# Performance work log

Measured on AMD Instinct MI355X. Metric: run time of the kernel, lower is better.

## Reference

```python
import jax, jax.numpy as jnp
import numpy as np
jax.config.update("jax_enable_x64", True)

B, S, E, H, L, FF = 2, 1024, 768, 12, 4, 2048
MAX_THOUGHT_LEN = 3
LN_EPS = 1e-5

def _sinusoidal_pe(max_len, d):
    pos = np.arange(max_len)[:, None]
    div = np.exp(np.arange(0, d, 2) * (-np.log(10000.0) / d))
    pe = np.zeros((max_len, d), np.float32)
    pe[:, 0::2] = np.sin(pos * div)
    pe[:, 1::2] = np.cos(pos * div)
    return jnp.asarray(pe)

def _build_mask(Smax, thoughts_taken, n_tokens):
    # Vectorized equivalent of the torch loop building the block-causal mask.
    bs = thoughts_taken + 1
    i = np.arange(Smax)[:, None]
    j = np.arange(Smax)[None, :]
    same_block = (i // bs == j // bs) & (i // bs < n_tokens) & ((i % bs) >= (j % bs))
    start_vis = ((j % bs) == 0) & (j // bs < n_tokens) & (i > j) & (i < n_tokens * bs)
    allowed = same_block | start_vis
    # TransformerEncoder canonicalizes the bool mask: True (disallowed) -> -inf additive
    return jnp.asarray(np.where(allowed, 0.0, -np.inf).astype(np.float64))

def _layernorm(x, w, b):
    mu = jnp.mean(x, -1, keepdims=True)
    var = jnp.mean((x - mu) ** 2, -1, keepdims=True)
    return (x - mu) / jnp.sqrt(var + LN_EPS) * w + b

def setup_inputs() -> dict:
    key = jax.random.key(0)
    ks = jax.random.split(key, 8)
    f32 = jnp.float32
    return {
        "x": jax.random.normal(ks[0], (B, S, E), f32),
        "padding_mask": jnp.zeros((B, S), bool),
        "thought_pe": jax.random.normal(ks[1], (MAX_THOUGHT_LEN + 1, E), f32),
        "Wqkv": jax.random.normal(ks[2], (L, 3 * E, E), f32) * (E ** -0.5),
        "bqkv": jnp.zeros((L, 3 * E), f32),
        "W1": jax.random.normal(ks[3], (L, FF, E), f32) * (E ** -0.5),
        "b1": jnp.zeros((L, FF), f32),
        "W2": jax.random.normal(ks[4], (L, E, FF), f32) * (FF ** -0.5),
        "b2": jnp.zeros((L, E), f32),
        "ln1_w": jnp.ones((L, E), f32), "ln1_b": jnp.zeros((L, E), f32),
        "ln2_w": jnp.ones((L, E), f32), "ln2_b": jnp.zeros((L, E), f32),
        "lnf_w": jnp.ones((E,), f32), "lnf_b": jnp.zeros((E,), f32),
        "thoughts_taken": 1,
        "real_token_count": 512,
    }

def reference(x, padding_mask, thought_pe, Wqkv, bqkv, W1, b1, W2, b2,
              ln1_w, ln1_b, ln2_w, ln2_b, lnf_w, lnf_b,
              thoughts_taken, real_token_count):
    # NOTE: padding_mask is accepted but unused, matching the custom layer.
    nt = thoughts_taken + 1
    pe = _sinusoidal_pe(S, E)
    # DualPositionalEncoding (eval mode -> dropout is identity)
    h = x[:, : real_token_count * nt].reshape(B, real_token_count, nt, E)
    h = h + pe[:real_token_count][None, :, None, :] + thought_pe[:nt][None, None, :, :]
    h = h.reshape(B, real_token_count * nt, E)
    pad = S - real_token_count * nt
    if pad > 0:
        h = jnp.pad(h, ((0, 0), (0, pad), (0, 0)))
    mask = _build_mask(S, thoughts_taken, real_token_count)
    scale = 1.0 / jnp.sqrt(jnp.float64(E // H))
    for l in range(L):
        # manual fp64 attention, exactly as the torch layer
        s64 = h.astype(jnp.float64)
        qkv = s64 @ Wqkv[l].astype(jnp.float64).T + bqkv[l].astype(jnp.float64)
        q, k, v = jnp.split(qkv, 3, axis=-1)
        rh = lambda t: t.reshape(B, S, H, E // H).transpose(0, 2, 1, 3)
        q, k, v = rh(q), rh(k), rh(v)
        scores = jnp.einsum("bhqd,bhkd->bhqk", q, k) * scale + mask
        attn = jax.nn.softmax(scores, axis=-1)
        ao = jnp.einsum("bhqk,bhkd->bhqd", attn, v).transpose(0, 2, 1, 3).reshape(B, S, E)
        # NOTE: no out_proj -- the custom forward skips self_attn.out_proj
        h = _layernorm(h + ao.astype(h.dtype), ln1_w[l], ln1_b[l])
        ff = jax.nn.gelu(h @ W1[l].T + b1[l], approximate=False) @ W2[l].T + b2[l]
        h = _layernorm(h + ff, ln2_w[l], ln2_b[l])
        h = jnp.nan_to_num(h)
    return _layernorm(h, lnf_w, lnf_b)
```

## Files before the change

kernel.cpp:

```cpp
#include <hip/hip_runtime.h>
#include <math.h>

#define SEQ 1024
#define EMB 768
#define NHEAD 12
#define HDIM 64
#define NLAYER 4
#define FFDIM 2048
#define BATCH 2
#define ROWS (BATCH * SEQ)
#define BH (BATCH * NHEAD)
#define NCHUNK 2
#define CTILES 8

using f16 = _Float16;
using f16x4 = __attribute__((ext_vector_type(4))) _Float16;
using f16x8 = __attribute__((ext_vector_type(8))) _Float16;
using f32x4 = __attribute__((ext_vector_type(4))) float;
using f32x16 = __attribute__((ext_vector_type(16))) float;
typedef unsigned long long u64;

__device__ inline void gload16(const void* g, void* l) {
    __builtin_amdgcn_global_load_lds((const __attribute__((address_space(1))) unsigned*)g,
                                     (__attribute__((address_space(3))) unsigned*)l, 16, 0, 0);
}

__global__ void prep_kernel(const float* __restrict__ Wq, int na,
                            const float* __restrict__ W1, int nb,
                            const float* __restrict__ W2, int nc,
                            f16* __restrict__ oq, f16* __restrict__ o1, f16* __restrict__ o2,
                            const float* __restrict__ x,
                            const float* __restrict__ tpe,
                            float* __restrict__ h32,
                            f16* __restrict__ h16,
                            u64* __restrict__ mtab,
                            const int* __restrict__ tt_p,
                            const int* __restrict__ rtc_p) {
    const int ncast = na + nb + nc;
    const int nembed = BATCH * SEQ * EMB;
    const int nmask = SEQ * 16;
    const int total = ncast + nembed + nmask;
    const int nt = *tt_p + 1;
    const int rtc = *rtc_p;
    for (int i = blockIdx.x * blockDim.x + threadIdx.x; i < total;
         i += gridDim.x * blockDim.x) {
        if (i < ncast) {
            const float* src;
            f16* dst;
            int off;
            if (i < na)            { src = Wq; dst = oq; off = i; }
            else if (i < na + nb)  { src = W1; dst = o1; off = i - na; }
            else                   { src = W2; dst = o2; off = i - na - nb; }
            float4 v = ((const float4*)src)[off];
            f16x4 o;
            o[0] = (f16)v.x; o[1] = (f16)v.y; o[2] = (f16)v.z; o[3] = (f16)v.w;
            ((f16x4*)dst)[off] = o;
        } else if (i < ncast + nembed) {
            int idx = i - ncast;
            int e = idx % EMB;
            int s = (idx / EMB) % SEQ;
            float val;
            if (s < rtc * nt) {
                int p = s / nt;
                int t = s % nt;
                int i2 = e & ~1;
                float div = __expf((float)i2 * -0.0119926314f);
                float ang = (float)p * div;
                float pe = (e & 1) ? __cosf(ang) : __sinf(ang);
                val = x[idx] + pe + tpe[t * EMB + e];
            } else {
                val = 0.0f;
            }
            h32[idx] = val;
            h16[idx] = (f16)val;
        } else {
            int idx = i - ncast - nembed;
            int ii = idx >> 4, jt = idx & 15;
            int id = ii / nt, im = ii % nt;
            int iok = (ii < rtc * nt);
            u64 m = 0;
            for (int k = 0; k < 64; k++) {
                int j = jt * 64 + k;
                int jd = j / nt, jm = j % nt;
                bool same = (id == jd) && (id < rtc) && (im >= jm);
                bool sv   = (jm == 0) && (jd < rtc) && (ii > j) && iok;
                if (same || sv) m |= (1ull << k);
            }
            mtab[idx] = m;
        }
    }
}

template<int ACT, int OUT>
__global__ __launch_bounds__(512) void gemm_f16(const f16* __restrict__ A,
                                                const f16* __restrict__ W,
                                                const float* __restrict__ bias,
                                                f16* __restrict__ Ch,
                                                f16* __restrict__ vtg,
                                                int M, int N, int K) {
    __shared__ f16 As[2][128 * 64];
    __shared__ f16 Ws[2][128 * 64];
    const int tid = threadIdx.x, lane = tid & 63, wave = tid >> 6;
    const int gx = gridDim.x;
    const int nwg = gx * gridDim.y;
    int orig = blockIdx.y * gx + blockIdx.x;
    int nid = (nwg & 7) ? orig : ((orig & 7) * (nwg >> 3) + (orig >> 3));
    const int bm = (nid / gx) * 128, bn = (nid % gx) * 128;
    const int l31 = lane & 31, l32 = lane >> 5;
    const int wm = (wave >> 1) * 32, wn = (wave & 1) * 64;
    const int srow = lane >> 3, sslot = lane & 7;
    const int klen = K / gridDim.z;
    const int kbeg = blockIdx.z * klen;
    const int nsteps = klen >> 6;

    f32x16 acc[2];
#pragma unroll
    for (int ni = 0; ni < 2; ni++)
#pragma unroll
        for (int e = 0; e < 16; e++) acc[ni][e] = 0.f;

#pragma unroll
    for (int i = 0; i < 2; i++) {
        int R0 = wave * 16 + i * 8;
        int row = R0 + srow;
        int gs = (sslot ^ (row & 7)) << 3;
        gload16(A + (size_t)(bm + row) * K + kbeg + gs, As[0] + R0 * 64);
        gload16(W + (size_t)(bn + row) * K + kbeg + gs, Ws[0] + R0 * 64);
    }
    __syncthreads();

    int cur = 0;
    for (int t = 0; t < nsteps; t++) {
        if (t + 1 < nsteps) {
            int k1 = kbeg + (t + 1) * 64;
            int nxt = cur ^ 1;
#pragma unroll
            for (int i = 0; i < 2; i++) {
                int R0 = wave * 16 + i * 8;
                int row = R0 + srow;
                int gs = (sslot ^ (row & 7)) << 3;
                gload16(A + (size_t)(bm + row) * K + k1 + gs, As[nxt] + R0 * 64);
                gload16(W + (size_t)(bn + row) * K + k1 + gs, Ws[nxt] + R0 * 64);
            }
        }
#pragma unroll
        for (int ks = 0; ks < 4; ks++) {
            int kslot = ks * 2 + l32;
            f16x8 a, b[2];
            {
                int row = wm + l31;
                a = *(const f16x8*)(As[cur] + row * 64 + ((kslot ^ (row & 7)) << 3));
            }
#pragma unroll
            for (int ni = 0; ni < 2; ni++) {
                int row = wn + ni * 32 + l31;
                b[ni] = *(const f16x8*)(Ws[cur] + row * 64 + ((kslot ^ (row & 7)) << 3));
            }
#pragma unroll
            for (int ni = 0; ni < 2; ni++)
                acc[ni] = __builtin_amdgcn_mfma_f32_32x32x16_f16(a, b[ni], acc[ni], 0, 0, 0);
        }
        __syncthreads();
        cur ^= 1;
    }

#pragma unroll
    for (int ni = 0; ni < 2; ni++) {
        int nbase = bn + wn + ni * 32;
        int n = nbase + l31;
        if (OUT == 3) {
            f16* dst = Ch + (size_t)blockIdx.z * ROWS * N;
#pragma unroll
            for (int reg = 0; reg < 16; reg++) {
                int m = bm + wm + (reg & 3) + 8 * (reg >> 2) + 4 * l32;
                dst[(size_t)m * N + n] = (f16)acc[ni][reg];
            }
        } else {
            float bv = bias[n];
            if (OUT != 2 || nbase < 2 * EMB) {
                int cstride = (OUT == 2) ? 2 * EMB : N;
#pragma unroll
                for (int reg = 0; reg < 16; reg++) {
                    int m = bm + wm + (reg & 3) + 8 * (reg >> 2) + 4 * l32;
                    float v = acc[ni][reg] + bv;
                    if (ACT) v = 0.5f * v * (1.0f + erff(v * 0.70710678118654752f));
                    Ch[(size_t)m * cstride + n] = (f16)v;
                }
            } else {
                int d = n - 2 * EMB;
                int hh = d >> 6, dd = d & 63;
#pragma unroll
                for (int q = 0; q < 4; q++) {
                    int m0 = bm + wm + 8 * q + 4 * l32;
                    int bb = m0 >> 10, s0 = m0 & (SEQ - 1);
                    f16x4 pack;
#pragma unroll
                    for (int r = 0; r < 4; r++) pack[r] = (f16)(acc[ni][4 * q + r] + bv);
                    *(f16x4*)(vtg + ((size_t)((bb * NHEAD + hh) * HDIM + dd)) * SEQ + s0) = pack;
                }
            }
        }
    }
}

__global__ __launch_bounds__(256) void attn_part(const f16* __restrict__ qk,
                                                 const f16* __restrict__ vtg,
                                                 const u64* __restrict__ mtab,
                                                 f16* __restrict__ po,
                                                 float* __restrict__ pm,
                                                 float* __restrict__ pl) {
    const int c = blockIdx.x;
    const int qt = gridDim.y - 1 - blockIdx.y;
    if (c * CTILES > qt) return;
    const int bh = blockIdx.z;
    const int b = bh / NHEAD, hh = bh % NHEAD;
    const int q0 = qt * 64;
    const int jt_beg = c * CTILES, jt_end = min(qt, c * CTILES + CTILES - 1);

    __shared__ f16 Qs[64 * 64];
    __shared__ f16 Ks[2][64 * 64];
    __shared__ f16 VT[2][64 * 64];
    __shared__ f16 Ps[4 * 16 * 64];

    const int tid = threadIdx.x, lane = tid & 63, wave = tid >> 6;
    const int l15 = lane & 15, l16 = lane >> 4;
    const int RS = 2 * EMB;
    const f16* vth = vtg + (size_t)(b * NHEAD + hh) * HDIM * SEQ;
    const float SCALE2 = 0.125f * 1.44269504088896f;

#pragma unroll
    for (int it = 0; it < 2; it++) {
        int R0 = wave * 16 + it * 8;
        int row = R0 + (lane >> 3), slot = lane & 7;
        int gs = (slot ^ (row & 7)) << 3;
        gload16(qk + (size_t)(b * SEQ + q0 + row) * RS + hh * HDIM + gs, Qs + R0 * 64);
        gload16(qk + (size_t)(b * SEQ + jt_beg * 64 + row) * RS + EMB + hh * HDIM + gs,
                Ks[0] + R0 * 64);
        gload16(vth + (size_t)row * SEQ + jt_beg * 64 + gs, VT[0] + R0 * 64);
    }
    __syncthreads();

    f16x8 qa[2];
#pragma unroll
    for (int ks = 0; ks < 2; ks++) {
        int row = wave * 16 + l15;
        int kslot = l16 + ks * 4;
        qa[ks] = *(const f16x8*)(Qs + row * 64 + ((kslot ^ (row & 7)) << 3));
    }

    f16x8 ones;
#pragma unroll
    for (int i = 0; i < 8; i++) ones[i] = (f16)1.0f;

    float mrow[4];
    f32x4 o[4], osum;
    int iglob[4];
#pragma unroll
    for (int r = 0; r < 4; r++) {
        mrow[r] = -1e30f;
        iglob[r] = q0 + wave * 16 + l16 * 4 + r;
    }
#pragma unroll
    for (int nf = 0; nf < 4; nf++) o[nf] = (f32x4){0.f, 0.f, 0.f, 0.f};
    osum = (f32x4){0.f, 0.f, 0.f, 0.f};

    for (int jt = jt_beg; jt <= jt_end; jt++) {
        const int cur = (jt - jt_beg) & 1;
        if (jt < jt_end) {
            const int nxt = cur ^ 1;
            const int jn0 = (jt + 1) * 64;
#pragma unroll
            for (int it = 0; it < 2; it++) {
                int R0 = wave * 16 + it * 8;
                int row = R0 + (lane >> 3), slot = lane & 7;
                int gs = (slot ^ (row & 7)) << 3;
                gload16(qk + (size_t)(b * SEQ + jn0 + row) * RS + EMB + hh * HDIM + gs,
                        Ks[nxt] + R0 * 64);
                gload16(vth + (size_t)row * SEQ + jn0 + gs, VT[nxt] + R0 * 64);
            }
        }

        unsigned mlo[4], mhi[4];
#pragma unroll
        for (int r = 0; r < 4; r++) {
            u64 mk = mtab[iglob[r] * 16 + jt];
            mlo[r] = (unsigned)mk;
            mhi[r] = (unsigned)(mk >> 32);
        }

        f32x4 s[4];
        __builtin_amdgcn_s_setprio(1);
#pragma unroll
        for (int nf = 0; nf < 4; nf++) {
            s[nf] = (f32x4){0.f, 0.f, 0.f, 0.f};
#pragma unroll
            for (int ks = 0; ks < 2; ks++) {
                int row = nf * 16 + l15;
                int kslot = l16 + ks * 4;
                f16x8 kb = *(const f16x8*)(Ks[cur] + row * 64 + ((kslot ^ (row & 7)) << 3));
                s[nf] = __builtin_amdgcn_mfma_f32_16x16x32_f16(qa[ks], kb, s[nf], 0, 0, 0);
            }
        }
        __builtin_amdgcn_s_setprio(0);

        float p[4][4];
        float tmax[4] = {-1e30f, -1e30f, -1e30f, -1e30f};
#pragma unroll
        for (int nf = 0; nf < 4; nf++) {
            int sh = (nf & 1) * 16 + l15;
#pragma unroll
            for (int r = 0; r < 4; r++) {
                unsigned w = (nf & 2) ? mhi[r] : mlo[r];
                bool allowed = (w >> sh) & 1;
                float val = allowed ? s[nf][r] * SCALE2 : -1e30f;
                p[nf][r] = val;
                tmax[r] = fmaxf(tmax[r], val);
            }
        }
#pragma unroll
        for (int r = 0; r < 4; r++) {
            tmax[r] = fmaxf(tmax[r], __shfl_xor(tmax[r], 1));
            tmax[r] = fmaxf(tmax[r], __shfl_xor(tmax[r], 2));
            tmax[r] = fmaxf(tmax[r], __shfl_xor(tmax[r], 4));
            tmax[r] = fmaxf(tmax[r], __shfl_xor(tmax[r], 8));
        }
        float alpha[4], meff[4];
#pragma unroll
        for (int r = 0; r < 4; r++) {
            float mn = fmaxf(mrow[r], tmax[r]);
            alpha[r] = exp2f(mrow[r] - mn);
            mrow[r] = mn;
            meff[r] = (mn <= -1e29f) ? 0.f : mn;
        }
#pragma unroll
        for (int nf = 0; nf < 4; nf++)
#pragma unroll
            for (int r = 0; r < 4; r++)
                p[nf][r] = exp2f(p[nf][r] - meff[r]);
#pragma unroll
        for (int r = 0; r < 4; r++) osum[r] *= alpha[r];
#pragma unroll
        for (int nf = 0; nf < 4; nf++)
#pragma unroll
            for (int r = 0; r < 4; r++) o[nf][r] *= alpha[r];

        f16* P = Ps + wave * 16 * 64;
#pragma unroll
        for (int nf = 0; nf < 4; nf++)
#pragma unroll
            for (int r = 0; r < 4; r++) {
                int prow = l16 * 4 + r;
                int pcol = nf * 16 + l15;
                P[prow * 64 + (((pcol >> 3) ^ (prow & 7)) << 3) + (pcol & 7)] = (f16)p[nf][r];
            }

        __builtin_amdgcn_s_setprio(1);
#pragma unroll
        for (int ks = 0; ks < 2; ks++) {
            int kslot = l16 + ks * 4;
            int prow = l15;
            f16x8 pa = *(const f16x8*)(P + prow * 64 + ((kslot ^ (prow & 7)) << 3));
            osum = __builtin_amdgcn_mfma_f32_16x16x32_f16(pa, ones, osum, 0, 0, 0);
#pragma unroll
            for (int nf = 0; nf < 4; nf++) {
                int vrow = nf * 16 + l15;
                f16x8 vb = *(const f16x8*)(VT[cur] + vrow * 64 + ((kslot ^ (vrow & 7)) << 3));
                o[nf] = __builtin_amdgcn_mfma_f32_16x16x32_f16(pa, vb, o[nf], 0, 0, 0);
            }
        }
        __builtin_amdgcn_s_setprio(0);
        __syncthreads();
    }

    const size_t base = (size_t)(c * BH + bh) * SEQ;
#pragma unroll
    for (int r = 0; r < 4; r++) {
        int i = q0 + wave * 16 + l16 * 4 + r;
#pragma unroll
        for (int nf = 0; nf < 4; nf++)
            po[(base + i) * 64 + nf * 16 + l15] = (f16)o[nf][r];
        if (l15 == 0) {
            pm[base + i] = mrow[r];
            pl[base + i] = osum[r];
        }
    }
}

__global__ __launch_bounds__(256) void add_ln_attn(const float* __restrict__ X,
                                                   const f16* __restrict__ po,
                                                   const float* __restrict__ pm,
                                                   const float* __restrict__ pl,
                                                   const float* __restrict__ w,
                                                   const float* __restrict__ bsh,
                                                   float* __restrict__ out32,
                                                   f16* __restrict__ out16) {
    const int row = blockIdx.x * 4 + (threadIdx.x >> 6);
    const int lane = threadIdx.x & 63;
    const int b = row >> 10, i = row & (SEQ - 1);
    const int nch = (i >> 6) / CTILES + 1;
    const float* xr = X + (size_t)row * EMB;
    float4 v[3];
    float s = 0.f;
#pragma unroll
    for (int t = 0; t < 3; t++) {
        int e = t * 256 + lane * 4;
        int hh = e >> 6, d = e & 63;
        size_t hbase = (size_t)(b * NHEAD + hh) * SEQ + i;
        float m = -1e30f;
        for (int c = 0; c < nch; c++) m = fmaxf(m, pm[hbase + (size_t)c * BH * SEQ]);
        float meff = (m <= -1e29f) ? 0.f : m;
        float lt = 0.f;
        float4 ov = {0.f, 0.f, 0.f, 0.f};
        for (int c = 0; c < nch; c++) {
            size_t idx = hbase + (size_t)c * BH * SEQ;
            float wgt = exp2f(pm[idx] - meff);
            lt += pl[idx] * wgt;
            f16x4 pv = *(const f16x4*)(po + idx * 64 + d);
            ov.x += (float)pv[0] * wgt; ov.y += (float)pv[1] * wgt;
            ov.z += (float)pv[2] * wgt; ov.w += (float)pv[3] * wgt;
        }
        float inv = (lt > 0.f) ? 1.0f / lt : 0.0f;
        float4 a = *(const float4*)(xr + e);
        a.x += ov.x * inv; a.y += ov.y * inv; a.z += ov.z * inv; a.w += ov.w * inv;
        v[t] = a;
        s += a.x + a.y + a.z + a.w;
    }
#pragma unroll
    for (int k = 1; k < 64; k <<= 1) s += __shfl_xor(s, k);
    float mu = s * (1.0f / EMB);
    float s2 = 0.f;
#pragma unroll
    for (int t = 0; t < 3; t++) {
        float dx = v[t].x - mu, dy = v[t].y - mu, dz = v[t].z - mu, dw = v[t].w - mu;
        s2 += dx * dx + dy * dy + dz * dz + dw * dw;
    }
#pragma unroll
    for (int k = 1; k < 64; k <<= 1) s2 += __shfl_xor(s2, k);
    float inv = rsqrtf(s2 * (1.0f / EMB) + 1e-5f);
#pragma unroll
    for (int t = 0; t < 3; t++) {
        int e = t * 256 + lane * 4;
        float4 wv = *(const float4*)(w + e);
        float4 bv = *(const float4*)(bsh + e);
        float4 o;
        o.x = (v[t].x - mu) * inv * wv.x + bv.x;
        o.y = (v[t].y - mu) * inv * wv.y + bv.y;
        o.z = (v[t].z - mu) * inv * wv.z + bv.z;
        o.w = (v[t].w - mu) * inv * wv.w + bv.w;
        *(float4*)(out32 + (size_t)row * EMB + e) = o;
        f16x4 hh;
        hh[0] = (f16)o.x; hh[1] = (f16)o.y; hh[2] = (f16)o.z; hh[3] = (f16)o.w;
        *(f16x4*)(out16 + (size_t)row * EMB + e) = hh;
    }
}

template<int FINAL>
__global__ __launch_bounds__(256) void add_ln_split4(const float* __restrict__ X,
                                                     const f16* __restrict__ part,
                                                     const float* __restrict__ bias,
                                                     const float* __restrict__ w,
                                                     const float* __restrict__ bsh,
                                                     const float* __restrict__ wf,
                                                     const float* __restrict__ bf,
                                                     float* __restrict__ out32,
                                                     f16* __restrict__ out16) {
    const int row = blockIdx.x * 4 + (threadIdx.x >> 6);
    const int lane = threadIdx.x & 63;
    const float* xr = X + (size_t)row * EMB;
    float4 v[3];
    float s = 0.f;
#pragma unroll
    for (int t = 0; t < 3; t++) {
        int e = t * 256 + lane * 4;
        float4 a = *(const float4*)(xr + e);
        float4 bb = *(const float4*)(bias + e);
        a.x += bb.x; a.y += bb.y; a.z += bb.z; a.w += bb.w;
#pragma unroll
        for (int z = 0; z < 4; z++) {
            f16x4 pz = *(const f16x4*)(part + (size_t)z * ROWS * EMB + (size_t)row * EMB + e);
            a.x += (float)pz[0]; a.y += (float)pz[1];
            a.z += (float)pz[2]; a.w += (float)pz[3];
        }
        v[t] = a;
        s += a.x + a.y + a.z + a.w;
    }
#pragma unroll
    for (int k = 1; k < 64; k <<= 1) s += __shfl_xor(s, k);
    float mu = s * (1.0f / EMB);
    float s2 = 0.f;
#pragma unroll
    for (int t = 0; t < 3; t++) {
        float dx = v[t].x - mu, dy = v[t].y - mu, dz = v[t].z - mu, dw = v[t].w - mu;
        s2 += dx * dx + dy * dy + dz * dz + dw * dw;
    }
#pragma unroll
    for (int k = 1; k < 64; k <<= 1) s2 += __shfl_xor(s2, k);
    float inv = rsqrtf(s2 * (1.0f / EMB) + 1e-5f);
    float4 o2[3];
    float sF = 0.f;
#pragma unroll
    for (int t = 0; t < 3; t++) {
        int e = t * 256 + lane * 4;
        float4 wv = *(const float4*)(w + e);
        float4 bv = *(const float4*)(bsh + e);
        float4 o;
        o.x = (v[t].x - mu) * inv * wv.x + bv.x;
        o.y = (v[t].y - mu) * inv * wv.y + bv.y;
        o.z = (v[t].z - mu) * inv * wv.z + bv.z;
        o.w = (v[t].w - mu) * inv * wv.w + bv.w;
        o2[t] = o;
        if (FINAL) sF += o.x + o.y + o.z + o.w;
        else {
            *(float4*)(out32 + (size_t)row * EMB + e) = o;
            f16x4 hh;
            hh[0] = (f16)o.x; hh[1] = (f16)o.y; hh[2] = (f16)o.z; hh[3] = (f16)o.w;
            *(f16x4*)(out16 + (size_t)row * EMB + e) = hh;
        }
    }
    if (FINAL) {
#pragma unroll
        for (int k = 1; k < 64; k <<= 1) sF += __shfl_xor(sF, k);
        float muF = sF * (1.0f / EMB);
        float s2F = 0.f;
#pragma unroll
        for (int t = 0; t < 3; t++) {
            float dx = o2[t].x - muF, dy = o2[t].y - muF, dz = o2[t].z - muF, dw = o2[t].w - muF;
            s2F += dx * dx + dy * dy + dz * dz + dw * dw;
        }
#pragma unroll
        for (int k = 1; k < 64; k <<= 1) s2F += __shfl_xor(s2F, k);
        float invF = rsqrtf(s2F * (1.0f / EMB) + 1e-5f);
#pragma unroll
        for (int t = 0; t < 3; t++) {
            int e = t * 256 + lane * 4;
            float4 wv = *(const float4*)(wf + e);
            float4 bv = *(const float4*)(bf + e);
            float4 o;
            o.x = (o2[t].x - muF) * invF * wv.x + bv.x;
            o.y = (o2[t].y - muF) * invF * wv.y + bv.y;
            o.z = (o2[t].z - muF) * invF * wv.z + bv.z;
            o.w = (o2[t].w - muF) * invF * wv.w + bv.w;
            *(float4*)(out32 + (size_t)row * EMB + e) = o;
        }
    }
}

extern "C" void kernel_launch(void* const* d_in, const int* in_sizes, int n_in,
                              void* d_out, int out_size, void* d_ws, size_t ws_size,
                              hipStream_t stream) {
    const float* x      = (const float*)d_in[0];
    const float* tpe    = (const float*)d_in[2];
    const float* Wqkv   = (const float*)d_in[3];
    const float* bqkv   = (const float*)d_in[4];
    const float* W1     = (const float*)d_in[5];
    const float* b1     = (const float*)d_in[6];
    const float* W2     = (const float*)d_in[7];
    const float* b2     = (const float*)d_in[8];
    const float* ln1_w  = (const float*)d_in[9];
    const float* ln1_b  = (const float*)d_in[10];
    const float* ln2_w  = (const float*)d_in[11];
    const float* ln2_b  = (const float*)d_in[12];
    const float* lnf_w  = (const float*)d_in[13];
    const float* lnf_b  = (const float*)d_in[14];
    const int*   tt     = (const int*)d_in[15];
    const int*   rtc    = (const int*)d_in[16];
    float* out = (float*)d_out;

    char* wsp = (char*)d_ws;
    float* h32  = (float*)wsp;
    f16*   h16  = (f16*)(wsp + 6291456);
    f16*   act  = (f16*)(wsp + 9437184);
    f16*   vtg  = (f16*)(wsp + 17825792);
    f16*   part = (f16*)(wsp + 20971520);
    f16*   wbuf = (f16*)(wsp + 33554432);
    f16*   po   = (f16*)(wsp + 72876032);
    float* pm   = (float*)(wsp + 79167488);
    float* pl   = (float*)(wsp + 79364096);
    u64*   mtab = (u64*)(wsp + 79560704);

    const int EQ = 3 * EMB * EMB;
    const int E1 = FFDIM * EMB;
    const int E2 = EMB * FFDIM;
    f16* wqAll = wbuf;
    f16* w1All = wbuf + (size_t)NLAYER * EQ;
    f16* w2All = w1All + (size_t)NLAYER * E1;

    prep_kernel<<<4096, 256, 0, stream>>>(Wqkv, NLAYER * EQ / 4, W1, NLAYER * E1 / 4,
                                          W2, NLAYER * E2 / 4, wqAll, w1All, w2All,
                                          x, tpe, h32, h16, mtab, tt, rtc);

    for (int l = 0; l < NLAYER; l++) {
        const f16* wq16 = wqAll + (size_t)l * EQ;
        const f16* w116 = w1All + (size_t)l * E1;
        const f16* w216 = w2All + (size_t)l * E2;
        const float* bq  = bqkv + (size_t)l * 3 * EMB;
        const float* bb1 = b1 + (size_t)l * FFDIM;
        const float* bb2 = b2 + (size_t)l * EMB;

        gemm_f16<0, 2><<<dim3(3 * EMB / 128, ROWS / 128), 512, 0, stream>>>(
            h16, wq16, bq, act, vtg, ROWS, 3 * EMB, EMB);

        attn_part<<<dim3(NCHUNK, SEQ / 64, BH), 256, 0, stream>>>(act, vtg, mtab, po, pm, pl);

        add_ln_attn<<<ROWS / 4, 256, 0, stream>>>(h32, po, pm, pl,
                                                  ln1_w + l * EMB, ln1_b + l * EMB, h32, h16);

        gemm_f16<1, 1><<<dim3(FFDIM / 128, ROWS / 128), 512, 0, stream>>>(
            h16, w116, bb1, act, nullptr, ROWS, FFDIM, EMB);

        gemm_f16<0, 3><<<dim3(EMB / 128, ROWS / 128, 4), 512, 0, stream>>>(
            act, w216, nullptr, part, nullptr, ROWS, EMB, FFDIM);

        if (l < NLAYER - 1)
            add_ln_split4<0><<<ROWS / 4, 256, 0, stream>>>(h32, part, bb2,
                ln2_w + l * EMB, ln2_b + l * EMB, nullptr, nullptr, h32, h16);
        else
            add_ln_split4<1><<<ROWS / 4, 256, 0, stream>>>(h32, part, bb2,
                ln2_w + l * EMB, ln2_b + l * EMB, lnf_w, lnf_b, out, nullptr);
    }
}
```

Baseline: 386.2 us.

## Drop split-KV attention chunks and halve FFN2 split-K partitions

The attention kernel stops splitting the key range into chunks: each block now walks all key tiles up to its query tile and normalises its output itself. That removes the partial max and sum buffers and the merge step in the attention layernorm kernel. The second FFN GEMM also goes from four split-K partitions to two, which cuts partial-sum traffic in the residual layernorm kernel. In exchange the grids are smaller and the causal attention blocks are more unbalanced, so occupancy and tail effects may get worse.

```diff
diff --git a/kernel.cpp b/kernel.cpp
--- a/kernel.cpp
+++ b/kernel.cpp
@@ -10,8 +10,6 @@
 #define BATCH 2
 #define ROWS (BATCH * SEQ)
 #define BH (BATCH * NHEAD)
-#define NCHUNK 2
-#define CTILES 8
 
 using f16 = _Float16;
 using f16x4 = __attribute__((ext_vector_type(4))) _Float16;
@@ -206,16 +204,11 @@
 __global__ __launch_bounds__(256) void attn_part(const f16* __restrict__ qk,
                                                  const f16* __restrict__ vtg,
                                                  const u64* __restrict__ mtab,
-                                                 f16* __restrict__ po,
-                                                 float* __restrict__ pm,
-                                                 float* __restrict__ pl) {
-    const int c = blockIdx.x;
-    const int qt = gridDim.y - 1 - blockIdx.y;
-    if (c * CTILES > qt) return;
-    const int bh = blockIdx.z;
+                                                 f16* __restrict__ po) {
+    const int qt = gridDim.x - 1 - blockIdx.x;
+    const int bh = blockIdx.y;
     const int b = bh / NHEAD, hh = bh % NHEAD;
     const int q0 = qt * 64;
-    const int jt_beg = c * CTILES, jt_end = min(qt, c * CTILES + CTILES - 1);
 
     __shared__ f16 Qs[64 * 64];
     __shared__ f16 Ks[2][64 * 64];
@@ -234,9 +227,8 @@
         int row = R0 + (lane >> 3), slot = lane & 7;
         int gs = (slot ^ (row & 7)) << 3;
         gload16(qk + (size_t)(b * SEQ + q0 + row) * RS + hh * HDIM + gs, Qs + R0 * 64);
-        gload16(qk + (size_t)(b * SEQ + jt_beg * 64 + row) * RS + EMB + hh * HDIM + gs,
-                Ks[0] + R0 * 64);
-        gload16(vth + (size_t)row * SEQ + jt_beg * 64 + gs, VT[0] + R0 * 64);
+        gload16(qk + (size_t)(b * SEQ + row) * RS + EMB + hh * HDIM + gs, Ks[0] + R0 * 64);
+        gload16(vth + (size_t)row * SEQ + gs, VT[0] + R0 * 64);
     }
     __syncthreads();
 
@@ -264,9 +256,9 @@
     for (int nf = 0; nf < 4; nf++) o[nf] = (f32x4){0.f, 0.f, 0.f, 0.f};
     osum = (f32x4){0.f, 0.f, 0.f, 0.f};
 
-    for (int jt = jt_beg; jt <= jt_end; jt++) {
-        const int cur = (jt - jt_beg) & 1;
-        if (jt < jt_end) {
+    for (int jt = 0; jt <= qt; jt++) {
+        const int cur = jt & 1;
+        if (jt < qt) {
             const int nxt = cur ^ 1;
             const int jn0 = (jt + 1) * 64;
 #pragma unroll
@@ -372,24 +364,19 @@
         __syncthreads();
     }
 
-    const size_t base = (size_t)(c * BH + bh) * SEQ;
+    const size_t base = (size_t)bh * SEQ;
 #pragma unroll
     for (int r = 0; r < 4; r++) {
         int i = q0 + wave * 16 + l16 * 4 + r;
+        float inv = (osum[r] > 0.f) ? 1.0f / osum[r] : 0.0f;
 #pragma unroll
         for (int nf = 0; nf < 4; nf++)
-            po[(base + i) * 64 + nf * 16 + l15] = (f16)o[nf][r];
-        if (l15 == 0) {
-            pm[base + i] = mrow[r];
-            pl[base + i] = osum[r];
-        }
+            po[(base + i) * 64 + nf * 16 + l15] = (f16)(o[nf][r] * inv);
     }
 }
 
 __global__ __launch_bounds__(256) void add_ln_attn(const float* __restrict__ X,
                                                    const f16* __restrict__ po,
-                                                   const float* __restrict__ pm,
-                                                   const float* __restrict__ pl,
                                                    const float* __restrict__ w,
                                                    const float* __restrict__ bsh,
                                                    float* __restrict__ out32,
@@ -397,7 +384,6 @@
     const int row = blockIdx.x * 4 + (threadIdx.x >> 6);
     const int lane = threadIdx.x & 63;
     const int b = row >> 10, i = row & (SEQ - 1);
-    const int nch = (i >> 6) / CTILES + 1;
     const float* xr = X + (size_t)row * EMB;
     float4 v[3];
     float s = 0.f;
@@ -405,23 +391,10 @@
     for (int t = 0; t < 3; t++) {
         int e = t * 256 + lane * 4;
         int hh = e >> 6, d = e & 63;
-        size_t hbase = (size_t)(b * NHEAD + hh) * SEQ + i;
-        float m = -1e30f;
-        for (int c = 0; c < nch; c++) m = fmaxf(m, pm[hbase + (size_t)c * BH * SEQ]);
-        float meff = (m <= -1e29f) ? 0.f : m;
-        float lt = 0.f;
-        float4 ov = {0.f, 0.f, 0.f, 0.f};
-        for (int c = 0; c < nch; c++) {
-            size_t idx = hbase + (size_t)c * BH * SEQ;
-            float wgt = exp2f(pm[idx] - meff);
-            lt += pl[idx] * wgt;
-            f16x4 pv = *(const f16x4*)(po + idx * 64 + d);
-            ov.x += (float)pv[0] * wgt; ov.y += (float)pv[1] * wgt;
-            ov.z += (float)pv[2] * wgt; ov.w += (float)pv[3] * wgt;
-        }
-        float inv = (lt > 0.f) ? 1.0f / lt : 0.0f;
+        f16x4 pv = *(const f16x4*)(po + ((size_t)(b * NHEAD + hh) * SEQ + i) * 64 + d);
         float4 a = *(const float4*)(xr + e);
-        a.x += ov.x * inv; a.y += ov.y * inv; a.z += ov.z * inv; a.w += ov.w * inv;
+        a.x += (float)pv[0]; a.y += (float)pv[1];
+        a.z += (float)pv[2]; a.w += (float)pv[3];
         v[t] = a;
         s += a.x + a.y + a.z + a.w;
     }
@@ -455,15 +428,15 @@
 }
 
 template<int FINAL>
-__global__ __launch_bounds__(256) void add_ln_split4(const float* __restrict__ X,
-                                                     const f16* __restrict__ part,
-                                                     const float* __restrict__ bias,
-                                                     const float* __restrict__ w,
-                                                     const float* __restrict__ bsh,
-                                                     const float* __restrict__ wf,
-                                                     const float* __restrict__ bf,
-                                                     float* __restrict__ out32,
-                                                     f16* __restrict__ out16) {
+__global__ __launch_bounds__(256) void add_ln_split(const float* __restrict__ X,
+                                                    const f16* __restrict__ part,
+                                                    const float* __restrict__ bias,
+                                                    const float* __restrict__ w,
+                                                    const float* __restrict__ bsh,
+                                                    const float* __restrict__ wf,
+                                                    const float* __restrict__ bf,
+                                                    float* __restrict__ out32,
+                                                    f16* __restrict__ out16) {
     const int row = blockIdx.x * 4 + (threadIdx.x >> 6);
     const int lane = threadIdx.x & 63;
     const float* xr = X + (size_t)row * EMB;
@@ -476,7 +449,7 @@
         float4 bb = *(const float4*)(bias + e);
         a.x += bb.x; a.y += bb.y; a.z += bb.z; a.w += bb.w;
 #pragma unroll
-        for (int z = 0; z < 4; z++) {
+        for (int z = 0; z < 2; z++) {
             f16x4 pz = *(const f16x4*)(part + (size_t)z * ROWS * EMB + (size_t)row * EMB + e);
             a.x += (float)pz[0]; a.y += (float)pz[1];
             a.z += (float)pz[2]; a.w += (float)pz[3];
@@ -572,11 +545,9 @@
     f16*   act  = (f16*)(wsp + 9437184);
     f16*   vtg  = (f16*)(wsp + 17825792);
     f16*   part = (f16*)(wsp + 20971520);
-    f16*   wbuf = (f16*)(wsp + 33554432);
-    f16*   po   = (f16*)(wsp + 72876032);
-    float* pm   = (float*)(wsp + 79167488);
-    float* pl   = (float*)(wsp + 79364096);
-    u64*   mtab = (u64*)(wsp + 79560704);
+    f16*   wbuf = (f16*)(wsp + 27262976);
+    f16*   po   = (f16*)(wsp + 66584576);
+    u64*   mtab = (u64*)(wsp + 69730304);
 
     const int EQ = 3 * EMB * EMB;
     const int E1 = FFDIM * EMB;
@@ -600,22 +571,22 @@
         gemm_f16<0, 2><<<dim3(3 * EMB / 128, ROWS / 128), 512, 0, stream>>>(
             h16, wq16, bq, act, vtg, ROWS, 3 * EMB, EMB);
 
-        attn_part<<<dim3(NCHUNK, SEQ / 64, BH), 256, 0, stream>>>(act, vtg, mtab, po, pm, pl);
-
-        add_ln_attn<<<ROWS / 4, 256, 0, stream>>>(h32, po, pm, pl,
+        attn_part<<<dim3(SEQ / 64, BH), 256, 0, stream>>>(act, vtg, mtab, po);
+
+        add_ln_attn<<<ROWS / 4, 256, 0, stream>>>(h32, po,
                                                   ln1_w + l * EMB, ln1_b + l * EMB, h32, h16);
 
         gemm_f16<1, 1><<<dim3(FFDIM / 128, ROWS / 128), 512, 0, stream>>>(
             h16, w116, bb1, act, nullptr, ROWS, FFDIM, EMB);
 
-        gemm_f16<0, 3><<<dim3(EMB / 128, ROWS / 128, 4), 512, 0, stream>>>(
+        gemm_f16<0, 3><<<dim3(EMB / 128, ROWS / 128, 2), 512, 0, stream>>>(
             act, w216, nullptr, part, nullptr, ROWS, EMB, FFDIM);
 
         if (l < NLAYER - 1)
-            add_ln_split4<0><<<ROWS / 4, 256, 0, stream>>>(h32, part, bb2,
+            add_ln_split<0><<<ROWS / 4, 256, 0, stream>>>(h32, part, bb2,
                 ln2_w + l * EMB, ln2_b + l * EMB, nullptr, nullptr, h32, h16);
         else
-            add_ln_split4<1><<<ROWS / 4, 256, 0, stream>>>(h32, part, bb2,
+            add_ln_split<1><<<ROWS / 4, 256, 0, stream>>>(h32, part, bb2,
                 ln2_w + l * EMB, ln2_b + l * EMB, lnf_w, lnf_b, out, nullptr);
     }
 }
```

New measurement: 428.5 us. 1.11x slower.
